# Kernel tuning notes

Measured on AMD Instinct MI355X. Metric: run time of the kernel, lower is better.

The kernel has to match this reference:

```python
import jax, jax.numpy as jnp
import numpy as np

D_MODEL = 1024
EXPANDED = 1024  # d_model * expansion_factor(1.0)
K = 3
EPS = 1e-8


def rms_norm(x, w, eps=EPS):
    return x * jax.lax.rsqrt(jnp.mean(x * x, axis=-1, keepdims=True) + eps) * w


def setup_inputs() -> dict:
    key = jax.random.key(0)
    ks = jax.random.split(key, 8)
    b, t = 4, 4096
    u = jax.random.normal(ks[0], (b, t, D_MODEL), dtype=jnp.float32)
    s_in = 1.0 / np.sqrt(D_MODEL)
    s_out = 1.0 / np.sqrt(EXPANDED)
    W_in = jax.random.uniform(ks[1], (2 * EXPANDED, D_MODEL), jnp.float32, -s_in, s_in)
    b_in = jax.random.uniform(ks[2], (2 * EXPANDED,), jnp.float32, -s_in, s_in)
    in_norm_w = jnp.ones((2 * EXPANDED,), jnp.float32)
    s_conv = 1.0 / np.sqrt(K)  # groups=expanded_dim -> fan_in = K
    conv_w = jax.random.uniform(ks[3], (EXPANDED, 1, K), jnp.float32, -s_conv, s_conv)
    conv_b = jax.random.uniform(ks[4], (EXPANDED,), jnp.float32, -s_conv, s_conv)
    W_out = jax.random.uniform(ks[5], (D_MODEL, EXPANDED), jnp.float32, -s_out, s_out)
    b_out = jax.random.uniform(ks[6], (D_MODEL,), jnp.float32, -s_out, s_out)
    out_norm_w = jnp.ones((D_MODEL,), jnp.float32)
    return {
        "u": u, "W_in": W_in, "b_in": b_in, "in_norm_w": in_norm_w,
        "conv_w": conv_w, "conv_b": conv_b,
        "W_out": W_out, "b_out": b_out, "out_norm_w": out_norm_w,
    }


def reference(u, W_in, b_in, in_norm_w, conv_w, conv_b, W_out, b_out, out_norm_w):
    # in_proj + RMSNorm
    xv = rms_norm(jnp.einsum('btd,ed->bte', u, W_in) + b_in, in_norm_w)  # [b,t,2E]
    x, v = jnp.split(xv, 2, axis=-1)  # each [b,t,E]
    # depthwise 'same' conv along time: NCH layout
    x_f = jnp.transpose(x, (0, 2, 1))  # [b,E,t]
    pad = (K - 1) // 2
    y = jax.lax.conv_general_dilated(
        x_f, conv_w, window_strides=(1,), padding=[(pad, pad)],
        dimension_numbers=('NCH', 'OIH', 'NCH'), feature_group_count=EXPANDED)
    y = y + conv_b[None, :, None]
    x_mixed = jnp.transpose(y, (0, 2, 1))  # [b,t,E]
    gated = v * x_mixed
    out = rms_norm(jnp.einsum('bte,de->btd', gated, W_out) + b_out, out_norm_w)
    return out
```

## Files before the change

kernel.cpp:

```cpp
#include <hip/hip_runtime.h>

#define BT    16384
#define TSEQ  4096
#define DM    1024
#define EXP   1024
#define N1    2048
#define KDIM  1024
#define NKT2  (KDIM / 32)
#define EPSV  1e-8f

typedef __bf16 bf16x8 __attribute__((ext_vector_type(8)));
typedef float f32x16 __attribute__((ext_vector_type(16)));
typedef unsigned short u16x8 __attribute__((ext_vector_type(8)));

#define AS1CAST(p) ((__attribute__((address_space(1))) void*)(p))
#define AS3CAST(p) ((__attribute__((address_space(3))) void*)(p))

__device__ __forceinline__ unsigned short f2bf(float f) {
    unsigned int u = __float_as_uint(f);
    u += 0x7fffu + ((u >> 16) & 1u);
    return (unsigned short)(u >> 16);
}

__global__ __launch_bounds__(256) void k_f2bf3(const float* __restrict__ i0, unsigned short* __restrict__ o0, int n0,
                                               const float* __restrict__ i1, unsigned short* __restrict__ o1, int n1,
                                               const float* __restrict__ i2, unsigned short* __restrict__ o2, int n2,
                                               float* __restrict__ ssq) {
    int i = blockIdx.x * 256 + threadIdx.x;
    const float* in; unsigned short* out;
    if (i < n0)                { in = i0; out = o0; }
    else if (i < n0 + n1)      { in = i1; out = o1; i -= n0; }
    else if (i < n0 + n1 + n2) { in = i2; out = o2; i -= n0 + n1; }
    else {
        i -= n0 + n1 + n2;
        if (i < 2 * BT / 4) ((float4*)ssq)[i] = make_float4(0.f, 0.f, 0.f, 0.f);
        return;
    }
    float4 v = ((const float4*)in)[i];
    ushort4 o;
    o.x = f2bf(v.x); o.y = f2bf(v.y); o.z = f2bf(v.z); o.w = f2bf(v.w);
    ((ushort4*)out)[i] = o;
}

template <int BF16_OUT, int NT>
__device__ __forceinline__ void gemm_body(const unsigned short* __restrict__ A,
                                          const unsigned short* __restrict__ Bw,
                                          const float* __restrict__ bias,
                                          unsigned short* __restrict__ Cb,
                                          float* __restrict__ Cf,
                                          float* __restrict__ ssq,
                                          int N) {
    __shared__ __align__(16) char smem[49152];
    unsigned short* sA0 = (unsigned short*)smem;
    unsigned short* sB0 = (unsigned short*)(smem + 16384);
    unsigned short* sA1 = (unsigned short*)(smem + 24576);
    unsigned short* sB1 = (unsigned short*)(smem + 40960);

    const int tid  = threadIdx.x;
    const int lane = tid & 63;
    const int w    = tid >> 6;
    const int ln   = lane & 31;
    const int hi   = lane >> 5;

    const int L   = blockIdx.x;
    const int mt  = ((L >> 3) / NT) * 8 + (L & 7);
    const int nt  = (L >> 3) & (NT - 1);
    const int row0 = mt * 256, col0 = nt * 128;

    const int rA = tid >> 2;
    const int qS = ((tid & 3) - rA) & 3;
    const unsigned short* aSrc = A  + (size_t)(row0 + rA) * KDIM + qS * 8;
    const unsigned short* bSrc = Bw + (size_t)(col0 + rA) * KDIM + qS * 8;

    f32x16 acc[2][4] = {};

    auto stage = [&](int kt, unsigned short* sA, unsigned short* sB) {
#pragma unroll
        for (int b = 0; b < 4; ++b)
            __builtin_amdgcn_global_load_lds(AS1CAST(aSrc + (size_t)b * 64 * KDIM + kt * 32),
                                             AS3CAST(&sA[(b * 256 + w * 64) * 8]), 16, 0, 0);
#pragma unroll
        for (int b = 0; b < 2; ++b)
            __builtin_amdgcn_global_load_lds(AS1CAST(bSrc + (size_t)b * 64 * KDIM + kt * 32),
                                             AS3CAST(&sB[(b * 256 + w * 64) * 8]), 16, 0, 0);
    };
    auto compute = [&](const unsigned short* sA, const unsigned short* sB) {
#pragma unroll
        for (int ks = 0; ks < 2; ++ks) {
            const int sw = ((ks * 2 + hi + ln) & 3) * 8;
            bf16x8 aF[2], bF[4];
#pragma unroll
            for (int i = 0; i < 2; ++i)
                aF[i] = *(const bf16x8*)&sA[(w * 64 + i * 32 + ln) * 32 + sw];
#pragma unroll
            for (int j = 0; j < 4; ++j)
                bF[j] = *(const bf16x8*)&sB[(j * 32 + ln) * 32 + sw];
#pragma unroll
            for (int i = 0; i < 2; ++i)
#pragma unroll
                for (int j = 0; j < 4; ++j)
                    acc[i][j] = __builtin_amdgcn_mfma_f32_32x32x16_bf16(
                        aF[i], bF[j], acc[i][j], 0, 0, 0);
        }
    };

    stage(0, sA0, sB0);
    for (int kt = 0; kt < NKT2; kt += 2) {
        __syncthreads();
        stage(kt + 1, sA1, sB1);
        compute(sA0, sB0);
        __syncthreads();
        if (kt + 2 < NKT2) stage(kt + 2, sA0, sB0);
        compute(sA1, sB1);
    }

    const int c0 = col0 + ln;
    float bs[4];
#pragma unroll
    for (int j = 0; j < 4; ++j) bs[j] = bias[c0 + j * 32];

    __syncthreads();
    float* scr = (float*)smem;

#pragma unroll
    for (int i = 0; i < 2; ++i) {
        const int lr0 = w * 64 + i * 32 + 4 * hi;
#pragma unroll
        for (int reg = 0; reg < 16; ++reg) {
            const int lr = lr0 + (reg & 3) + 8 * (reg >> 2);
            const int gm = row0 + lr;
            float v[4]; float p = 0.f;
#pragma unroll
            for (int j = 0; j < 4; ++j) {
                v[j] = acc[i][j][reg] + bs[j];
                p += v[j] * v[j];
            }
            scr[lr * 33 + ln] = p;
            size_t base = (size_t)gm * N + c0;
#pragma unroll
            for (int j = 0; j < 4; ++j) {
                if (BF16_OUT) Cb[base + j * 32] = f2bf(v[j]);
                else          Cf[base + j * 32] = v[j];
            }
        }
    }
    __syncthreads();
    float s = 0.f;
#pragma unroll
    for (int c = 0; c < 32; ++c) s += scr[tid * 33 + c];
    atomicAdd(&ssq[row0 + tid], s);
}

__global__ __launch_bounds__(256, 2) void k_gemm_in(const unsigned short* __restrict__ A,
                                                    const unsigned short* __restrict__ Bw,
                                                    const float* __restrict__ bias,
                                                    unsigned short* __restrict__ Cb,
                                                    float* __restrict__ ssq) {
    gemm_body<1, 16>(A, Bw, bias, Cb, nullptr, ssq, N1);
}

__global__ __launch_bounds__(256, 2) void k_gemm_out(const unsigned short* __restrict__ A,
                                                     const unsigned short* __restrict__ Bw,
                                                     const float* __restrict__ bias,
                                                     float* __restrict__ Cf,
                                                     float* __restrict__ ssq) {
    gemm_body<0, 8>(A, Bw, bias, nullptr, Cf, ssq, DM);
}

__global__ __launch_bounds__(256) void k_conv_gate(const unsigned short* __restrict__ z,
                                                   const float* __restrict__ ssq1,
                                                   const float* __restrict__ inw,
                                                   const float* __restrict__ cw,
                                                   const float* __restrict__ cb,
                                                   unsigned short* __restrict__ g) {
    const int tok = blockIdx.x * 2 + (threadIdx.x >> 7);
    const int e8  = (threadIdx.x & 127) * 8;
    const int t   = tok & (TSEQ - 1);

    const float rs0 = rsqrtf(ssq1[tok] * (1.0f / N1) + EPSV);
    const int tm = (t > 0) ? tok - 1 : tok;
    const int tp = (t < TSEQ - 1) ? tok + 1 : tok;
    const float rsm = (t > 0) ? rsqrtf(ssq1[tm] * (1.0f / N1) + EPSV) : 0.0f;
    const float rsp = (t < TSEQ - 1) ? rsqrtf(ssq1[tp] * (1.0f / N1) + EPSV) : 0.0f;

    bf16x8 xm = *(const bf16x8*)(z + (size_t)tm * N1 + e8);
    bf16x8 x0 = *(const bf16x8*)(z + (size_t)tok * N1 + e8);
    bf16x8 xp = *(const bf16x8*)(z + (size_t)tp * N1 + e8);
    bf16x8 vv = *(const bf16x8*)(z + (size_t)tok * N1 + EXP + e8);

    u16x8 ov;
#pragma unroll
    for (int p = 0; p < 8; ++p) {
        const int e = e8 + p;
        const float we  = inw[e];
        const float wvv = inw[EXP + e];
        const float w0 = cw[e * 3], w1 = cw[e * 3 + 1], w2 = cw[e * 3 + 2];
        float y = w0 * ((float)xm[p] * rsm * we)
                + w1 * ((float)x0[p] * rs0 * we)
                + w2 * ((float)xp[p] * rsp * we)
                + cb[e];
        float vn = (float)vv[p] * rs0 * wvv;
        ov[p] = f2bf(vn * y);
    }
    *(u16x8*)(g + (size_t)tok * EXP + e8) = ov;
}

__global__ __launch_bounds__(256) void k_outnorm(float* __restrict__ o,
                                                 const float* __restrict__ ssq2,
                                                 const float* __restrict__ onw) {
    const int idx = blockIdx.x * 256 + threadIdx.x;
    const int tok = idx >> 8;
    const int d4  = (idx & 255) * 4;
    const float rs = rsqrtf(ssq2[tok] * (1.0f / DM) + EPSV);
    float4 v = ((float4*)o)[idx];
    float4 w = *(const float4*)(onw + d4);
    v.x *= rs * w.x; v.y *= rs * w.y; v.z *= rs * w.z; v.w *= rs * w.w;
    ((float4*)o)[idx] = v;
}

extern "C" void kernel_launch(void* const* d_in, const int* in_sizes, int n_in,
                              void* d_out, int out_size, void* d_ws, size_t ws_size,
                              hipStream_t stream) {
    const float* u     = (const float*)d_in[0];
    const float* W_in  = (const float*)d_in[1];
    const float* b_in  = (const float*)d_in[2];
    const float* inw   = (const float*)d_in[3];
    const float* cw    = (const float*)d_in[4];
    const float* cb    = (const float*)d_in[5];
    const float* W_out = (const float*)d_in[6];
    const float* b_out = (const float*)d_in[7];
    const float* onw   = (const float*)d_in[8];
    float* out = (float*)d_out;

    char* ws = (char*)d_ws;
    unsigned short* u_bf    = (unsigned short*)ws; ws += (size_t)BT * DM * 2;
    unsigned short* Win_bf  = (unsigned short*)ws; ws += (size_t)N1 * DM * 2;
    unsigned short* Wout_bf = (unsigned short*)ws; ws += (size_t)DM * EXP * 2;
    unsigned short* z_bf    = (unsigned short*)ws; ws += (size_t)BT * N1 * 2;
    unsigned short* g_bf    = (unsigned short*)ws; ws += (size_t)BT * EXP * 2;
    float* ssq1 = (float*)ws; ws += (size_t)BT * 4;
    float* ssq2 = (float*)ws; ws += (size_t)BT * 4;

    const int n0 = BT * DM / 4, n1c = N1 * DM / 4, n2c = DM * EXP / 4;
    const int ntot = n0 + n1c + n2c + 2 * BT / 4;
    k_f2bf3<<<(ntot + 255) / 256, 256, 0, stream>>>(u, u_bf, n0,
                                                    W_in, Win_bf, n1c,
                                                    W_out, Wout_bf, n2c,
                                                    ssq1);

    k_gemm_in<<<(BT / 256) * (N1 / 128), 256, 0, stream>>>(u_bf, Win_bf, b_in, z_bf, ssq1);

    k_conv_gate<<<BT / 2, 256, 0, stream>>>(z_bf, ssq1, inw, cw, cb, g_bf);

    k_gemm_out<<<(BT / 256) * (DM / 128), 256, 0, stream>>>(g_bf, Wout_bf, b_out, out, ssq2);

    k_outnorm<<<BT, 256, 0, stream>>>(out, ssq2, onw);

    (void)in_sizes; (void)n_in; (void)out_size; (void)ws_size;
}
```

Before: 302.0 us.

## Triple-buffer GEMM LDS stages with explicit vmcnt waits and MFMA priority

Replaces the two-stage double-buffered K loop in the shared GEMM body with a three-buffer ring. Two tiles stay in flight, and each step waits with s_waitcnt vmcnt(6) plus a single barrier instead of two __syncthreads per pair of tiles. It also changes the LDS swizzle to key on row/4 instead of row, and raises wave priority around the MFMA block. The goal is to hide global-to-LDS latency and cut barrier stalls. The cost is LDS growing from 48KB to 72KB per block, which can lower occupancy.

Result: no change. 299.6 us (-0.8%).

```diff
diff --git a/kernel.cpp b/kernel.cpp
--- a/kernel.cpp
+++ b/kernel.cpp
@@ -6,7 +6,7 @@
 #define EXP   1024
 #define N1    2048
 #define KDIM  1024
-#define NKT2  (KDIM / 32)
+#define NKT   32
 #define EPSV  1e-8f
 
 typedef __bf16 bf16x8 __attribute__((ext_vector_type(8)));
@@ -50,11 +50,7 @@
                                           float* __restrict__ Cf,
                                           float* __restrict__ ssq,
                                           int N) {
-    __shared__ __align__(16) char smem[49152];
-    unsigned short* sA0 = (unsigned short*)smem;
-    unsigned short* sB0 = (unsigned short*)(smem + 16384);
-    unsigned short* sA1 = (unsigned short*)(smem + 24576);
-    unsigned short* sB1 = (unsigned short*)(smem + 40960);
+    __shared__ __align__(16) char smem[73728];
 
     const int tid  = threadIdx.x;
     const int lane = tid & 63;
@@ -68,7 +64,7 @@
     const int row0 = mt * 256, col0 = nt * 128;
 
     const int rA = tid >> 2;
-    const int qS = ((tid & 3) - rA) & 3;
+    const int qS = ((tid & 3) - (tid >> 4)) & 3;
     const unsigned short* aSrc = A  + (size_t)(row0 + rA) * KDIM + qS * 8;
     const unsigned short* bSrc = Bw + (size_t)(col0 + rA) * KDIM + qS * 8;
 
@@ -87,7 +83,7 @@
     auto compute = [&](const unsigned short* sA, const unsigned short* sB) {
 #pragma unroll
         for (int ks = 0; ks < 2; ++ks) {
-            const int sw = ((ks * 2 + hi + ln) & 3) * 8;
+            const int sw = ((ks * 2 + hi + (ln >> 2)) & 3) * 8;
             bf16x8 aF[2], bF[4];
 #pragma unroll
             for (int i = 0; i < 2; ++i)
@@ -95,24 +91,37 @@
 #pragma unroll
             for (int j = 0; j < 4; ++j)
                 bF[j] = *(const bf16x8*)&sB[(j * 32 + ln) * 32 + sw];
+            __builtin_amdgcn_s_setprio(1);
 #pragma unroll
             for (int i = 0; i < 2; ++i)
 #pragma unroll
                 for (int j = 0; j < 4; ++j)
                     acc[i][j] = __builtin_amdgcn_mfma_f32_32x32x16_bf16(
                         aF[i], bF[j], acc[i][j], 0, 0, 0);
+            __builtin_amdgcn_s_setprio(0);
         }
     };
 
-    stage(0, sA0, sB0);
-    for (int kt = 0; kt < NKT2; kt += 2) {
-        __syncthreads();
-        stage(kt + 1, sA1, sB1);
-        compute(sA0, sB0);
-        __syncthreads();
-        if (kt + 2 < NKT2) stage(kt + 2, sA0, sB0);
-        compute(sA1, sB1);
-    }
+    unsigned short* A0 = (unsigned short*)smem;
+    unsigned short* B0 = (unsigned short*)(smem + 16384);
+    unsigned short* A1 = (unsigned short*)(smem + 24576);
+    unsigned short* B1 = (unsigned short*)(smem + 40960);
+    unsigned short* A2 = (unsigned short*)(smem + 49152);
+    unsigned short* B2 = (unsigned short*)(smem + 65536);
+
+    stage(0, A0, B0);
+    stage(1, A1, B1);
+    for (int kt = 0; kt < NKT - 1; ++kt) {
+        asm volatile("s_waitcnt vmcnt(6)" ::: "memory");
+        __builtin_amdgcn_s_barrier();
+        if (kt + 2 < NKT) stage(kt + 2, A2, B2);
+        compute(A0, B0);
+        unsigned short* tA = A0; A0 = A1; A1 = A2; A2 = tA;
+        unsigned short* tB = B0; B0 = B1; B1 = B2; B2 = tB;
+    }
+    asm volatile("s_waitcnt vmcnt(0)" ::: "memory");
+    __builtin_amdgcn_s_barrier();
+    compute(A0, B0);
 
     const int c0 = col0 + ln;
     float bs[4];
```
